# Kernel tuning notes

Measured on AMD Instinct MI355X. Metric: run time of the kernel, lower is better.

Reference implementation:

```python
import jax, jax.numpy as jnp
import numpy as np

GRID_SIZE = 5
SPLINE_ORDER = 3
GRID_RANGE = (-1.0, 1.0)
BATCH, IN_FEATURES, OUT_FEATURES = 8192, 512, 512


def make_grid():
    h = (GRID_RANGE[1] - GRID_RANGE[0]) / GRID_SIZE
    n = GRID_SIZE + 2 * SPLINE_ORDER + 1  # 12 knots
    return jnp.linspace(GRID_RANGE[0] - SPLINE_ORDER * h,
                        GRID_RANGE[1] + SPLINE_ORDER * h,
                        n, dtype=jnp.float32)


def b_spline(x, grid, k=SPLINE_ORDER):
    # Cox-de Boor recursion. x: (B, in) -> basis: (B, in, grid_size + k)
    x = x[..., None]                     # (B, in, 1)
    g = grid[None, None, :]              # (1, 1, n_knots)
    basis = ((x >= g[..., :-1]) & (x < g[..., 1:])).astype(x.dtype)
    for p in range(1, k + 1):
        left_denom = g[..., p:-1] - g[..., :-(p + 1)]
        right_denom = g[..., p + 1:] - g[..., 1:-p]
        left_denom = jnp.where(left_denom > 0, left_denom, jnp.ones_like(left_denom))
        right_denom = jnp.where(right_denom > 0, right_denom, jnp.ones_like(right_denom))
        left = (x - g[..., :-(p + 1)]) / left_denom * basis[..., :-1]
        right = (g[..., p + 1:] - x) / right_denom * basis[..., 1:]
        basis = left + right
    return basis


def setup_inputs() -> dict:
    key = jax.random.key(0)
    k1, k2, k3 = jax.random.split(key, 3)
    # x uniform in grid_range so spline basis is active
    x = jax.random.uniform(k1, (BATCH, IN_FEATURES), jnp.float32, minval=-1.0, maxval=1.0)
    # kaiming_uniform-like init for base weight
    bound = 1.0 / np.sqrt(IN_FEATURES)
    base_weight = jax.random.uniform(k2, (OUT_FEATURES, IN_FEATURES), jnp.float32,
                                     minval=-bound, maxval=bound)
    spline_weight = jax.random.normal(k3, (OUT_FEATURES, IN_FEATURES,
                                           GRID_SIZE + SPLINE_ORDER), jnp.float32) * 0.1
    return {"x": x, "base_weight": base_weight, "spline_weight": spline_weight}


def reference(x, base_weight, spline_weight):
    grid = make_grid()
    scale_base, scale_spline = 1.0, 1.0
    base_out = x @ base_weight.T                         # (B, out)
    basis = b_spline(x, grid, SPLINE_ORDER)              # (B, in, G+k)
    spline_out = jnp.einsum('bil,oil->bo', basis, spline_weight)
    return scale_base * base_out + scale_spline * spline_out
```

## Files before the change

kernel.cpp:

```cpp
#include <hip/hip_runtime.h>
#include <stdint.h>

typedef _Float16 half8 __attribute__((ext_vector_type(8)));
typedef float floatx4 __attribute__((ext_vector_type(4)));
typedef uint32_t u32x4 __attribute__((ext_vector_type(4)));

#define BM 128
#define BN 128
#define BK 64
#define NT 512
#define KT_BASE 8
#define KT_TOTAL 72
#define KT_HALF 36
#define IF 512
#define NF 512
#define SW_K 4096
#define TILE_B 16384
#define WS_TILES (KT_TOTAL * 4)

__device__ __forceinline__ uint32_t swz(uint32_t b) {
  return b ^ (((b >> 7) & 7u) << 4);
}

__device__ __forceinline__ uint32_t pk(float a, float b) {
  return __builtin_bit_cast(uint32_t, __builtin_amdgcn_cvt_pkrtz(a, b));
}

__global__ __launch_bounds__(256)
void kan_zero(float4* __restrict__ p, int n4) {
  const int stride = gridDim.x * 256;
  for (int i = blockIdx.x * 256 + threadIdx.x; i < n4; i += stride)
    p[i] = (float4){0.f, 0.f, 0.f, 0.f};
}

__global__ __launch_bounds__(256)
void kan_prep(const float* __restrict__ bwg, const float* __restrict__ swg,
              uint32_t* __restrict__ wsB)
{
  const int gid = blockIdx.x * 256 + threadIdx.x;
  const int T = gid >> 10;
  const int q = gid & 1023;
  const int kt = T >> 2;
  const int nt = T & 3;
  const uint32_t p = swz((uint32_t)q * 16u);
  const int row = p >> 7;
  const int c   = (p & 127) >> 1;
  const int n = nt * 128 + row;
  const float* src;
  if (kt < KT_BASE) src = bwg + (size_t)n * IF   + kt * 64 + c;
  else              src = swg + (size_t)n * SW_K + (kt - KT_BASE) * 64 + c;
  float4 f0 = ((const float4*)src)[0];
  float4 f1 = ((const float4*)src)[1];
  u32x4 v; v.x = pk(f0.x, f0.y); v.y = pk(f0.z, f0.w);
           v.z = pk(f1.x, f1.y); v.w = pk(f1.z, f1.w);
  *(u32x4*)((char*)wsB + (size_t)T * TILE_B + (size_t)q * 16) = v;
}

__global__ __launch_bounds__(NT, 2)
void kan_fused(const float* __restrict__ xg, const uint32_t* __restrict__ wsB,
               float* __restrict__ outg)
{
  __shared__ _Float16 As[2][BM * BK];
  __shared__ _Float16 Bs[2][BN * BK];

  const int tid = threadIdx.x;
  const int lane = tid & 63;
  const int wv = tid >> 6;
  const int wm = wv >> 2;
  const int wn = wv & 3;

  const int bid = blockIdx.x;
  const int u = (bid & 7) * 64 + (bid >> 3);
  const int kz = u & 1;
  const int lb = u >> 1;
  const int bm0 = (lb & 63) * BM;
  const int ntI = lb >> 6;
  const int bn0 = ntI * BN;
  const int kt0 = kz * KT_HALF;
  const int kt1 = kt0 + KT_HALF;

  const int rT = tid >> 3;
  const int c8 = (tid & 7) * 8;
  const int ii = tid & 7;
  const uint32_t wA0 = swz((uint32_t)rT * 128u + (uint32_t)c8 * 2u);
  const uint32_t wA1 = swz((uint32_t)(rT + 64) * 128u + (uint32_t)c8 * 2u);

  char* AsB = (char*)As;
  char* BsB = (char*)Bs;

  uint32_t rdA[4], rdB[2];
  {
    const int rr = lane & 15;
    const uint32_t cc = (uint32_t)(lane >> 4) * 16u;
#pragma unroll
    for (int mi = 0; mi < 4; ++mi)
      rdA[mi] = swz((uint32_t)(wm * 64 + mi * 16 + rr) * 128u + cc);
#pragma unroll
    for (int ni = 0; ni < 2; ++ni)
      rdB[ni] = swz((uint32_t)(wn * 32 + ni * 16 + rr) * 128u + cc);
  }

  floatx4 acc[4][2];
#pragma unroll
  for (int mi = 0; mi < 4; ++mi)
#pragma unroll
    for (int ni = 0; ni < 2; ++ni)
      acc[mi][ni] = (floatx4){0.f, 0.f, 0.f, 0.f};

  float4 aL[4];
  float xv0, xv1;

  auto GLOADB = [&](int kt, int nb) {
    const char* src = (const char*)wsB + (size_t)(kt * 4 + ntI) * TILE_B + (size_t)tid * 16;
    char* dst = BsB + nb * TILE_B + tid * 16;
    __builtin_amdgcn_global_load_lds(
        (const __attribute__((address_space(1))) uint32_t*)src,
        (__attribute__((address_space(3))) uint32_t*)dst, 16, 0, 0);
    __builtin_amdgcn_global_load_lds(
        (const __attribute__((address_space(1))) uint32_t*)(src + 8192),
        (__attribute__((address_space(3))) uint32_t*)(dst + 8192), 16, 0, 0);
  };

  auto LOADX = [&](int kt) {
    if (kt < KT_BASE) {
      const int kb = kt * 64;
      const float* a0 = xg + (size_t)(bm0 + rT) * IF + kb + c8;
      const float* a1 = a0 + (size_t)64 * IF;
      aL[0] = ((const float4*)a0)[0]; aL[1] = ((const float4*)a0)[1];
      aL[2] = ((const float4*)a1)[0]; aL[3] = ((const float4*)a1)[1];
    } else {
      const int i0 = (kt - KT_BASE) * 8;
      xv0 = xg[(size_t)(bm0 + rT) * IF + i0 + ii];
      xv1 = xg[(size_t)(bm0 + rT + 64) * IF + i0 + ii];
    }
  };

  auto BASIS = [&](float xv) -> u32x4 {
    float u2 = (xv + 2.2f) * 2.5f;
    int j = (int)u2;
    j = j < 3 ? 3 : (j > 7 ? 7 : j);
    float t = u2 - (float)j;
    float omt = 1.0f - t;
    float t2 = t * t, t3 = t2 * t;
    const float s6 = 0.16666666666666666f;
    float w0 = omt * omt * omt * s6;
    float w1 = (3.0f * t3 - 6.0f * t2 + 4.0f) * s6;
    float w2 = (-3.0f * t3 + 3.0f * t2 + 3.0f * t + 1.0f) * s6;
    float w3 = t3 * s6;
    uint32_t c0 = pk(w0, w1);
    uint32_t c1 = pk(w2, w3);
    const int j3 = j - 3;
    const bool odd = (j3 & 1) != 0;
    uint32_t lo  = odd ? (c0 << 16) : c0;
    uint32_t mid = odd ? ((c0 >> 16) | (c1 << 16)) : c1;
    uint32_t hi  = odd ? (c1 >> 16) : 0u;
    const int wofs = j3 >> 1;
    u32x4 r;
    r.x = (wofs == 0) ? lo : 0u;
    r.y = (wofs == 0) ? mid : ((wofs == 1) ? lo : 0u);
    r.z = (wofs == 0) ? hi : ((wofs == 1) ? mid : lo);
    r.w = (wofs == 1) ? hi : ((wofs == 2) ? mid : 0u);
    return r;
  };

  auto WRITEA = [&](int kt, int nb) {
    char* base = AsB + nb * TILE_B;
    if (kt < KT_BASE) {
      u32x4 v0; v0.x = pk(aL[0].x, aL[0].y); v0.y = pk(aL[0].z, aL[0].w);
                v0.z = pk(aL[1].x, aL[1].y); v0.w = pk(aL[1].z, aL[1].w);
      u32x4 v1; v1.x = pk(aL[2].x, aL[2].y); v1.y = pk(aL[2].z, aL[2].w);
                v1.z = pk(aL[3].x, aL[3].y); v1.w = pk(aL[3].z, aL[3].w);
      *(u32x4*)(base + wA0) = v0;
      *(u32x4*)(base + wA1) = v1;
    } else {
      *(u32x4*)(base + wA0) = BASIS(xv0);
      *(u32x4*)(base + wA1) = BASIS(xv1);
    }
  };

  auto COMPUTE = [&](int cb) {
    const char* ab = AsB + cb * TILE_B;
    const char* bb = BsB + cb * TILE_B;
#pragma unroll
    for (int kk = 0; kk < 2; ++kk) {
      const uint32_t ko = (uint32_t)(kk * 64);
      half8 a[4], b[2];
#pragma unroll
      for (int mi = 0; mi < 4; ++mi)
        a[mi] = *(const half8*)(ab + (rdA[mi] ^ ko));
#pragma unroll
      for (int ni = 0; ni < 2; ++ni)
        b[ni] = *(const half8*)(bb + (rdB[ni] ^ ko));
#pragma unroll
      for (int mi = 0; mi < 4; ++mi)
#pragma unroll
        for (int ni = 0; ni < 2; ++ni)
          acc[mi][ni] = __builtin_amdgcn_mfma_f32_16x16x32_f16(a[mi], b[ni], acc[mi][ni], 0, 0, 0);
    }
  };

  LOADX(kt0);
  GLOADB(kt0, 0);
  WRITEA(kt0, 0);
  __syncthreads();

#pragma unroll 1
  for (int kt = kt0; kt < kt1; ++kt) {
    const int cur = kt & 1;
    const int nxt = cur ^ 1;
    const bool more = (kt + 1) < kt1;
    if (more) { GLOADB(kt + 1, nxt); LOADX(kt + 1); }
    COMPUTE(cur);
    if (more) WRITEA(kt + 1, nxt);
    __syncthreads();
  }

  const int er = (lane >> 4) * 4;
  const int ec = lane & 15;
#pragma unroll
  for (int mi = 0; mi < 4; ++mi) {
#pragma unroll
    for (int ni = 0; ni < 2; ++ni) {
      const size_t base = (size_t)(bm0 + wm * 64 + mi * 16 + er) * NF
                        + (size_t)(bn0 + wn * 32 + ni * 16 + ec);
#pragma unroll
      for (int e = 0; e < 4; ++e)
        unsafeAtomicAdd(outg + base + (size_t)e * NF, acc[mi][ni][e]);
    }
  }
}

extern "C" void kernel_launch(void* const* d_in, const int* in_sizes, int n_in,
                              void* d_out, int out_size, void* d_ws, size_t ws_size,
                              hipStream_t stream) {
  const float* x  = (const float*)d_in[0];
  const float* bw = (const float*)d_in[1];
  const float* sw = (const float*)d_in[2];
  float* out = (float*)d_out;
  uint32_t* wsB = (uint32_t*)d_ws;
  hipLaunchKernelGGL(kan_zero, dim3(2048), dim3(256), 0, stream, (float4*)out, out_size / 4);
  hipLaunchKernelGGL(kan_prep, dim3(WS_TILES * 1024 / 256), dim3(256), 0, stream, bw, sw, wsB);
  hipLaunchKernelGGL(kan_fused, dim3(512), dim3(NT), 0, stream, x, wsB, out);
}
```

Before: 88.44 us.

## Precompute swizzled fp16 A operand with B-spline basis in separate prep kernel

Moves the B-spline basis evaluation and fp16 conversion of x out of the GEMM main loop into a new kan_prepA kernel. That kernel writes pre-swizzled fp16 A tiles to workspace, chunked by rows when the workspace is too small. The GEMM then streams both A and B into LDS with global_load_lds, with no register staging or ALU work in the loop, and uses launch bounds of 4 for higher occupancy. The cost is an extra round trip through global memory for the expanded A matrix (about 75 MB of fp16) plus extra kernel launches.

```diff
diff --git a/kernel.cpp b/kernel.cpp
--- a/kernel.cpp
+++ b/kernel.cpp
@@ -5,25 +5,41 @@
 typedef float floatx4 __attribute__((ext_vector_type(4)));
 typedef uint32_t u32x4 __attribute__((ext_vector_type(4)));
 
-#define BM 128
-#define BN 128
-#define BK 64
-#define NT 512
-#define KT_BASE 8
-#define KT_TOTAL 72
-#define KT_HALF 36
 #define IF 512
 #define NF 512
-#define SW_K 4096
+#define KT_TOTAL 72
 #define TILE_B 16384
-#define WS_TILES (KT_TOTAL * 4)
+#define B_WS_BYTES ((size_t)KT_TOTAL * 4 * TILE_B)
 
 __device__ __forceinline__ uint32_t swz(uint32_t b) {
   return b ^ (((b >> 7) & 7u) << 4);
 }
-
 __device__ __forceinline__ uint32_t pk(float a, float b) {
   return __builtin_bit_cast(uint32_t, __builtin_amdgcn_cvt_pkrtz(a, b));
+}
+
+__device__ __forceinline__ u32x4 BASIS8(float xv) {
+  float u = (xv + 2.2f) * 2.5f;
+  float fj = __builtin_floorf(u);
+  fj = fminf(fmaxf(fj, 3.0f), 7.0f);
+  float t = u - fj;
+  float omt = 1.0f - t;
+  float t2 = t * t, t3 = t2 * t;
+  float w0 = omt * omt * omt * 0.16666666666666666f;
+  float w1 = __builtin_fmaf(0.5f, t3, 0.66666666666666666f - t2);
+  float w2 = __builtin_fmaf(0.5f, (t2 - t3) + t, 0.16666666666666666f);
+  float w3 = t3 * 0.16666666666666666f;
+  uint32_t c0 = pk(w0, w1);
+  uint32_t c1 = pk(w2, w3);
+  int j3 = (int)fj - 3;
+  int sh = j3 << 4;
+  uint64_t w = (uint64_t)c0 | ((uint64_t)c1 << 32);
+  uint64_t lo = (sh < 64) ? (w << sh) : 0ull;
+  uint64_t hi = (sh == 0) ? 0ull : ((sh < 64) ? (w >> (64 - sh)) : w);
+  u32x4 r;
+  r.x = (uint32_t)lo; r.y = (uint32_t)(lo >> 32);
+  r.z = (uint32_t)hi; r.w = (uint32_t)(hi >> 32);
+  return r;
 }
 
 __global__ __launch_bounds__(256)
@@ -34,8 +50,8 @@
 }
 
 __global__ __launch_bounds__(256)
-void kan_prep(const float* __restrict__ bwg, const float* __restrict__ swg,
-              uint32_t* __restrict__ wsB)
+void kan_prepB(const float* __restrict__ bwg, const float* __restrict__ swg,
+               uint8_t* __restrict__ wsB)
 {
   const int gid = blockIdx.x * 256 + threadIdx.x;
   const int T = gid >> 10;
@@ -46,44 +62,59 @@
   const int row = p >> 7;
   const int c   = (p & 127) >> 1;
   const int n = nt * 128 + row;
-  const float* src;
-  if (kt < KT_BASE) src = bwg + (size_t)n * IF   + kt * 64 + c;
-  else              src = swg + (size_t)n * SW_K + (kt - KT_BASE) * 64 + c;
+  const float* src = (kt < 8) ? bwg + (size_t)n * IF + kt * 64 + c
+                              : swg + (size_t)n * 4096 + (kt - 8) * 64 + c;
   float4 f0 = ((const float4*)src)[0];
   float4 f1 = ((const float4*)src)[1];
   u32x4 v; v.x = pk(f0.x, f0.y); v.y = pk(f0.z, f0.w);
            v.z = pk(f1.x, f1.y); v.w = pk(f1.z, f1.w);
-  *(u32x4*)((char*)wsB + (size_t)T * TILE_B + (size_t)q * 16) = v;
-}
-
-__global__ __launch_bounds__(NT, 2)
-void kan_fused(const float* __restrict__ xg, const uint32_t* __restrict__ wsB,
-               float* __restrict__ outg)
+  *(u32x4*)(wsB + (size_t)T * TILE_B + (size_t)q * 16) = v;
+}
+
+__global__ __launch_bounds__(256)
+void kan_prepA(const float* __restrict__ xg, uint8_t* __restrict__ wsA, int row0)
 {
-  __shared__ _Float16 As[2][BM * BK];
-  __shared__ _Float16 Bs[2][BN * BK];
-
-  const int tid = threadIdx.x;
-  const int lane = tid & 63;
-  const int wv = tid >> 6;
-  const int wm = wv >> 2;
-  const int wn = wv & 3;
-
+  const int gid = blockIdx.x * 256 + threadIdx.x;
+  const int bl = gid / 576;
+  const int c  = gid - bl * 576;
+  const int b  = row0 + bl;
+  u32x4 v;
+  if (c < 64) {
+    const float* s = xg + (size_t)b * IF + c * 8;
+    float4 f0 = ((const float4*)s)[0];
+    float4 f1 = ((const float4*)s)[1];
+    v.x = pk(f0.x, f0.y); v.y = pk(f0.z, f0.w);
+    v.z = pk(f1.x, f1.y); v.w = pk(f1.z, f1.w);
+  } else {
+    v = BASIS8(xg[(size_t)b * IF + (c - 64)]);
+  }
+  const int mt = bl >> 7;
+  const int r  = bl & 127;
+  const int kt = c >> 3;
+  const uint32_t lin = (uint32_t)r * 128u + (uint32_t)(c & 7) * 16u;
+  *(u32x4*)(wsA + (size_t)(mt * KT_TOTAL + kt) * TILE_B + swz(lin)) = v;
+}
+
+__global__ __launch_bounds__(512, 4)
+void kan_gemm(const uint8_t* __restrict__ wsA, const uint8_t* __restrict__ wsB,
+              float* __restrict__ outg, int row0, int mtBits)
+{
+  __shared__ _Float16 As[2][8192];
+  __shared__ _Float16 Bs[2][8192];
+
+  const int tid = threadIdx.x, lane = tid & 63, wv = tid >> 6;
+  const int wm = wv >> 2, wn = wv & 3;
+
+  const int cpx = gridDim.x >> 3;
   const int bid = blockIdx.x;
-  const int u = (bid & 7) * 64 + (bid >> 3);
+  const int u = (bid & 7) * cpx + (bid >> 3);
   const int kz = u & 1;
   const int lb = u >> 1;
-  const int bm0 = (lb & 63) * BM;
-  const int ntI = lb >> 6;
-  const int bn0 = ntI * BN;
-  const int kt0 = kz * KT_HALF;
-  const int kt1 = kt0 + KT_HALF;
-
-  const int rT = tid >> 3;
-  const int c8 = (tid & 7) * 8;
-  const int ii = tid & 7;
-  const uint32_t wA0 = swz((uint32_t)rT * 128u + (uint32_t)c8 * 2u);
-  const uint32_t wA1 = swz((uint32_t)(rT + 64) * 128u + (uint32_t)c8 * 2u);
+  const int mt  = lb & ((1 << mtBits) - 1);
+  const int ntI = lb >> mtBits;
+  const int bm0 = row0 + mt * 128;
+  const int bn0 = ntI * 128;
+  const int kt0 = kz * 36, kt1 = kt0 + 36;
 
   char* AsB = (char*)As;
   char* BsB = (char*)Bs;
@@ -107,75 +138,19 @@
     for (int ni = 0; ni < 2; ++ni)
       acc[mi][ni] = (floatx4){0.f, 0.f, 0.f, 0.f};
 
-  float4 aL[4];
-  float xv0, xv1;
-
-  auto GLOADB = [&](int kt, int nb) {
-    const char* src = (const char*)wsB + (size_t)(kt * 4 + ntI) * TILE_B + (size_t)tid * 16;
-    char* dst = BsB + nb * TILE_B + tid * 16;
-    __builtin_amdgcn_global_load_lds(
-        (const __attribute__((address_space(1))) uint32_t*)src,
-        (__attribute__((address_space(3))) uint32_t*)dst, 16, 0, 0);
-    __builtin_amdgcn_global_load_lds(
-        (const __attribute__((address_space(1))) uint32_t*)(src + 8192),
-        (__attribute__((address_space(3))) uint32_t*)(dst + 8192), 16, 0, 0);
-  };
-
-  auto LOADX = [&](int kt) {
-    if (kt < KT_BASE) {
-      const int kb = kt * 64;
-      const float* a0 = xg + (size_t)(bm0 + rT) * IF + kb + c8;
-      const float* a1 = a0 + (size_t)64 * IF;
-      aL[0] = ((const float4*)a0)[0]; aL[1] = ((const float4*)a0)[1];
-      aL[2] = ((const float4*)a1)[0]; aL[3] = ((const float4*)a1)[1];
-    } else {
-      const int i0 = (kt - KT_BASE) * 8;
-      xv0 = xg[(size_t)(bm0 + rT) * IF + i0 + ii];
-      xv1 = xg[(size_t)(bm0 + rT + 64) * IF + i0 + ii];
-    }
-  };
-
-  auto BASIS = [&](float xv) -> u32x4 {
-    float u2 = (xv + 2.2f) * 2.5f;
-    int j = (int)u2;
-    j = j < 3 ? 3 : (j > 7 ? 7 : j);
-    float t = u2 - (float)j;
-    float omt = 1.0f - t;
-    float t2 = t * t, t3 = t2 * t;
-    const float s6 = 0.16666666666666666f;
-    float w0 = omt * omt * omt * s6;
-    float w1 = (3.0f * t3 - 6.0f * t2 + 4.0f) * s6;
-    float w2 = (-3.0f * t3 + 3.0f * t2 + 3.0f * t + 1.0f) * s6;
-    float w3 = t3 * s6;
-    uint32_t c0 = pk(w0, w1);
-    uint32_t c1 = pk(w2, w3);
-    const int j3 = j - 3;
-    const bool odd = (j3 & 1) != 0;
-    uint32_t lo  = odd ? (c0 << 16) : c0;
-    uint32_t mid = odd ? ((c0 >> 16) | (c1 << 16)) : c1;
-    uint32_t hi  = odd ? (c1 >> 16) : 0u;
-    const int wofs = j3 >> 1;
-    u32x4 r;
-    r.x = (wofs == 0) ? lo : 0u;
-    r.y = (wofs == 0) ? mid : ((wofs == 1) ? lo : 0u);
-    r.z = (wofs == 0) ? hi : ((wofs == 1) ? mid : lo);
-    r.w = (wofs == 1) ? hi : ((wofs == 2) ? mid : 0u);
-    return r;
-  };
-
-  auto WRITEA = [&](int kt, int nb) {
-    char* base = AsB + nb * TILE_B;
-    if (kt < KT_BASE) {
-      u32x4 v0; v0.x = pk(aL[0].x, aL[0].y); v0.y = pk(aL[0].z, aL[0].w);
-                v0.z = pk(aL[1].x, aL[1].y); v0.w = pk(aL[1].z, aL[1].w);
-      u32x4 v1; v1.x = pk(aL[2].x, aL[2].y); v1.y = pk(aL[2].z, aL[2].w);
-                v1.z = pk(aL[3].x, aL[3].y); v1.w = pk(aL[3].z, aL[3].w);
-      *(u32x4*)(base + wA0) = v0;
-      *(u32x4*)(base + wA1) = v1;
-    } else {
-      *(u32x4*)(base + wA0) = BASIS(xv0);
-      *(u32x4*)(base + wA1) = BASIS(xv1);
-    }
+  auto STAGE = [&](int kt, int nb) {
+    const uint8_t* sa = wsA + (size_t)(mt * KT_TOTAL + kt) * TILE_B + (size_t)tid * 16;
+    const uint8_t* sb = wsB + (size_t)(kt * 4 + ntI) * TILE_B + (size_t)tid * 16;
+    char* da = AsB + nb * TILE_B + tid * 16;
+    char* db = BsB + nb * TILE_B + tid * 16;
+    __builtin_amdgcn_global_load_lds((const __attribute__((address_space(1))) uint32_t*)sa,
+                                     (__attribute__((address_space(3))) uint32_t*)da, 16, 0, 0);
+    __builtin_amdgcn_global_load_lds((const __attribute__((address_space(1))) uint32_t*)(sa + 8192),
+                                     (__attribute__((address_space(3))) uint32_t*)(da + 8192), 16, 0, 0);
+    __builtin_amdgcn_global_load_lds((const __attribute__((address_space(1))) uint32_t*)sb,
+                                     (__attribute__((address_space(3))) uint32_t*)db, 16, 0, 0);
+    __builtin_amdgcn_global_load_lds((const __attribute__((address_space(1))) uint32_t*)(sb + 8192),
+                                     (__attribute__((address_space(3))) uint32_t*)(db + 8192), 16, 0, 0);
   };
 
   auto COMPUTE = [&](int cb) {
@@ -199,19 +174,13 @@
     }
   };
 
-  LOADX(kt0);
-  GLOADB(kt0, 0);
-  WRITEA(kt0, 0);
+  STAGE(kt0, 0);
   __syncthreads();
-
 #pragma unroll 1
   for (int kt = kt0; kt < kt1; ++kt) {
-    const int cur = kt & 1;
-    const int nxt = cur ^ 1;
-    const bool more = (kt + 1) < kt1;
-    if (more) { GLOADB(kt + 1, nxt); LOADX(kt + 1); }
+    const int cur = (kt - kt0) & 1;
+    if (kt + 1 < kt1) STAGE(kt + 1, cur ^ 1);
     COMPUTE(cur);
-    if (more) WRITEA(kt + 1, nxt);
     __syncthreads();
   }
 
@@ -237,8 +206,17 @@
   const float* bw = (const float*)d_in[1];
   const float* sw = (const float*)d_in[2];
   float* out = (float*)d_out;
-  uint32_t* wsB = (uint32_t*)d_ws;
-  hipLaunchKernelGGL(kan_zero, dim3(2048), dim3(256), 0, stream, (float4*)out, out_size / 4);
-  hipLaunchKernelGGL(kan_prep, dim3(WS_TILES * 1024 / 256), dim3(256), 0, stream, bw, sw, wsB);
-  hipLaunchKernelGGL(kan_fused, dim3(512), dim3(NT), 0, stream, x, wsB, out);
-}
+  uint8_t* wsB = (uint8_t*)d_ws;
+  uint8_t* wsA = wsB + B_WS_BYTES;
+
+  int R = 8192;
+  while (R > 512 && B_WS_BYTES + (size_t)R * 4608 * 2 > ws_size) R >>= 1;
+  int mtBits = 31 - __builtin_clz(R / 128);
+
+  hipLaunchKernelGGL(kan_zero,  dim3(2048), dim3(256), 0, stream, (float4*)out, out_size / 4);
+  hipLaunchKernelGGL(kan_prepB, dim3(1152), dim3(256), 0, stream, bw, sw, wsB);
+  for (int r0 = 0; r0 < 8192; r0 += R) {
+    hipLaunchKernelGGL(kan_prepA, dim3(R * 576 / 256), dim3(256), 0, stream, x, wsA, r0);
+    hipLaunchKernelGGL(kan_gemm,  dim3(R / 16), dim3(512), 0, stream, wsA, wsB, out, r0, mtBits);
+  }
+}
```

Result: slower. 97.80 us (+10.6%).
